# Performance work log

Hardware: AMD Instinct MI355X
Metric: run time of the kernel (lower is better)

The kernel has to match this reference:

```python
import jax, jax.numpy as jnp
import numpy as np

DIM = 512
HEADS = 8
DIM_HEAD = 64
HIDDEN = HEADS * DIM_HEAD
SCALE = DIM_HEAD ** -0.5


def rmsnorm_ch(x, g):
    # F.normalize over channel dim (axis=1), then * g * sqrt(C)
    # x: [b, c, l], g: [c]
    n = jnp.maximum(jnp.linalg.norm(x, axis=1, keepdims=True), 1e-12)
    c = x.shape[1]
    return (x / n) * g[None, :, None] * (c ** 0.5)


def setup_inputs() -> dict:
    key = jax.random.key(0)
    ks = jax.random.split(key, 6)
    b, l = 8, 4096
    x = jax.random.normal(ks[0], (b, DIM, l), dtype=jnp.float32)
    g_in = jnp.ones((DIM,), dtype=jnp.float32)
    # conv1d kernel_size=1 == matmul; kaiming-ish init scale
    w_qkv = jax.random.normal(ks[1], (3 * HIDDEN, DIM), dtype=jnp.float32) * (1.0 / np.sqrt(DIM))
    w_out = jax.random.normal(ks[2], (DIM, HIDDEN), dtype=jnp.float32) * (1.0 / np.sqrt(HIDDEN))
    b_out = jax.random.normal(ks[3], (DIM,), dtype=jnp.float32) * 0.01
    g_out = jnp.ones((DIM,), dtype=jnp.float32)
    return {"x": x, "g_in": g_in, "w_qkv": w_qkv, "w_out": w_out, "b_out": b_out, "g_out": g_out}


def reference(x, g_in, w_qkv, w_out, b_out, g_out):
    b, c, l = x.shape
    residual = x
    xn = rmsnorm_ch(x, g_in)                       # [b, c, l]
    qkv = jnp.einsum('oc,bcl->bol', w_qkv, xn)     # [b, 3*hidden, l]
    q, k, v = jnp.split(qkv, 3, axis=1)            # each [b, hidden, l]
    def to_heads(t):
        return t.reshape(b, HEADS, DIM_HEAD, l)    # [b, h, d, l]
    q, k, v = to_heads(q), to_heads(k), to_heads(v)
    q = jax.nn.softmax(q, axis=2) * SCALE          # softmax over head-dim d
    k = jax.nn.softmax(k, axis=3)                  # softmax over sequence l
    context = jnp.einsum('bhdn,bhen->bhde', k, v)  # [b, h, d, e]
    out = jnp.einsum('bhde,bhdn->bhen', context, q)  # [b, h, e, l]
    out = out.reshape(b, HIDDEN, l)
    o = jnp.einsum('ch,bhl->bcl', w_out, out) + b_out[None, :, None]
    o = rmsnorm_ch(o, g_out)
    return o + residual
```

## Files before the change

### kernel.cpp

```cpp
#include <hip/hip_runtime.h>


#define BB 8
#define CC 512
#define LL 4096
#define HH 8
#define DH 64
#define TC 1536

__device__ __constant__ const float SQRT_C = 22.62741699796952f;
#define SCALE_Q 0.125f

typedef unsigned short bfr_t;
typedef __attribute__((ext_vector_type(8))) short short8;
typedef __attribute__((ext_vector_type(4))) float f32x4;

__device__ __forceinline__ float bf2f(bfr_t v) {
  union { unsigned u; float f; } c; c.u = ((unsigned)v) << 16; return c.f;
}
__device__ __forceinline__ bfr_t f2bf(float f) {
  union { float f; unsigned u; } c; c.f = f;
  unsigned u = c.u + 0x7fffu + ((c.u >> 16) & 1u);
  return (bfr_t)(u >> 16);
}

__device__ __forceinline__ void load_lds16(const bfr_t* g, short* l) {
  __builtin_amdgcn_global_load_lds(
      (const __attribute__((address_space(1))) void*)g,
      (__attribute__((address_space(3))) void*)l, 16, 0, 0);
}

__global__ __launch_bounds__(256) void conv_bf16_2(
    const float* __restrict__ in1, bfr_t* __restrict__ o1, int n1,
    const float* __restrict__ in2, bfr_t* __restrict__ o2, int n2) {
  int i8 = (blockIdx.x * 256 + threadIdx.x) * 8;
  const float* src;
  bfr_t* dst;
  if (i8 < n1) { src = in1 + i8; dst = o1 + i8; }
  else {
    int j8 = i8 - n1;
    if (j8 >= n2) return;
    src = in2 + j8; dst = o2 + j8;
  }
  f32x4 a = *(const f32x4*)src;
  f32x4 b = *(const f32x4*)(src + 4);
  union { short s[8]; f32x4 v; } pk;
#pragma unroll
  for (int u = 0; u < 4; ++u) { pk.s[u] = (short)f2bf(a[u]); pk.s[u + 4] = (short)f2bf(b[u]); }
  *(f32x4*)dst = pk.v;
}

__global__ __launch_bounds__(256) void fused_norm_transpose(
    const float* __restrict__ x, const float* __restrict__ g,
    bfr_t* __restrict__ xt) {
  __shared__ float tile[64][65];
  __shared__ float red[4][64];
  __shared__ float invn_s[64];
  int b = blockIdx.y, l0 = blockIdx.x * 64;
  int t = threadIdx.x, ll = t & 63, cg = t >> 6;
  const float* xb = x + (size_t)b * CC * LL + l0;
  float vals[8][16];
  float ss = 0.f;
#pragma unroll
  for (int ch = 0; ch < 8; ++ch) {
    int c0 = ch * 64;
#pragma unroll
    for (int i = 0; i < 16; ++i) {
      int c = i * 4 + cg;
      float v = xb[(size_t)(c0 + c) * LL + ll];
      vals[ch][i] = v;
      ss += v * v;
    }
  }
  red[cg][ll] = ss;
  __syncthreads();
  if (cg == 0) {
    float s = red[0][ll] + red[1][ll] + red[2][ll] + red[3][ll];
    invn_s[ll] = SQRT_C / fmaxf(sqrtf(s), 1e-12f);
  }
  __syncthreads();
  int lw = t >> 2, ccw = (t & 3) * 16;
  float iv = invn_s[lw];
#pragma unroll
  for (int ch = 0; ch < 8; ++ch) {
    int c0 = ch * 64;
#pragma unroll
    for (int i = 0; i < 16; ++i) tile[i * 4 + cg][ll] = vals[ch][i];
    __syncthreads();
    union { short s[16]; f32x4 v[2]; } pk;
#pragma unroll
    for (int u = 0; u < 16; ++u) {
      int c = ccw + u;
      pk.s[u] = (short)f2bf(tile[c][lw] * g[c0 + c] * iv);
    }
    bfr_t* dst = xt + ((size_t)b * LL + l0 + lw) * CC + c0 + ccw;
    *(f32x4*)dst = pk.v[0];
    *(f32x4*)(dst + 8) = pk.v[1];
    __syncthreads();
  }
}

#define NT 8

__device__ __forceinline__ void stage_half(const bfr_t* g, short* l, int wid) {
  load_lds16(g + (size_t)wid * 8192,        l + wid * 1024);
  load_lds16(g + (size_t)wid * 8192 + 4096, l + wid * 1024 + 512);
}

#define CFENCE asm volatile("" ::: "memory")
#define LGKM0 asm volatile("s_waitcnt lgkmcnt(0)" ::: "memory")
#define VMC0  asm volatile("s_waitcnt vmcnt(0)" ::: "memory")
#define SB    __builtin_amdgcn_sched_barrier(0)
#define BAR   do { CFENCE; __builtin_amdgcn_s_barrier(); CFENCE; } while (0)
#define PRIO1 __builtin_amdgcn_s_setprio(1)
#define PRIO0 __builtin_amdgcn_s_setprio(0)

#define DSR(dst, addr, LIT) \
  asm volatile("ds_read_b128 %0, %1 offset:" #LIT : "=v"(dst) : "v"(addr))

#define RD_A(S, L0, L1, L2, L3) do {           \
    DSR(S[0], aAs0, L0); DSR(S[1], aAs1, L0);  \
    DSR(S[2], aAs0, L1); DSR(S[3], aAs1, L1);  \
    DSR(S[4], aAs0, L2); DSR(S[5], aAs1, L2);  \
    DSR(S[6], aAs0, L3); DSR(S[7], aAs1, L3); } while (0)
#define RD_B(S, L0, L1) do {                   \
    DSR(S[0], bBs0, L0); DSR(S[1], bBs1, L0);  \
    DSR(S[2], bBs0, L1); DSR(S[3], bBs1, L1); } while (0)

#define MMA8(QM, QN, AS, BS) do {                                            \
    _Pragma("unroll") for (int i_ = 0; i_ < 4; ++i_)                         \
      _Pragma("unroll") for (int j_ = 0; j_ < 2; ++j_) {                     \
        acc[(QM)*4+i_][(QN)*2+j_] = __builtin_amdgcn_mfma_f32_16x16x32_bf16( \
            AS[i_*2+0], BS[j_*2+0], acc[(QM)*4+i_][(QN)*2+j_], 0, 0, 0);     \
        acc[(QM)*4+i_][(QN)*2+j_] = __builtin_amdgcn_mfma_f32_16x16x32_bf16( \
            AS[i_*2+1], BS[j_*2+1], acc[(QM)*4+i_][(QN)*2+j_], 0, 0, 0);     \
      }                                                                      \
  } while (0)

#define STAGE_T(J, D) do {                                                   \
    stage_half(pA0 + (J) * 64, As + (D) * 16384, wid);                       \
    stage_half(pA1 + (J) * 64, As + (D) * 16384 + 8192, wid);                \
    stage_half(pB0 + (J) * 64, Bs + (D) * 16384, wid);                       \
    stage_half(pB1 + (J) * 64, Bs + (D) * 16384 + 8192, wid);                \
  } while (0)

#define TILE_E(KT) do {                                                      \
                                      \
    PRIO1; RD_B(bS1, 4096, 6144); MMA8(0, 0, aS0, bS0); PRIO0; LGKM0; SB;    \
                                      \
    PRIO1; RD_A(aS1, 8192, 10240, 12288, 14336); MMA8(0, 1, aS0, bS1);       \
    PRIO0; LGKM0; SB;                                                        \
         \
    if ((KT) < 7) { VMC0; }                                                  \
    BAR;                                                                     \
    if ((KT) <= 5) STAGE_T((KT) + 2, 0);                                     \
    PRIO1;                                                                   \
    if ((KT) < 7) RD_A(aS0, 32768, 34816, 36864, 38912);                     \
    MMA8(1, 1, aS1, bS1); PRIO0; LGKM0; SB;                                  \
            \
    PRIO1; MMA8(1, 0, aS1, bS0); PRIO0;                                      \
    if ((KT) < 7) RD_B(bS0, 32768, 34816);                                   \
    LGKM0; SB;                                                               \
  } while (0)

#define TILE_O(KT) do {                                                      \
    PRIO1; RD_B(bS1, 36864, 38912); MMA8(0, 0, aS0, bS0); PRIO0; LGKM0; SB;  \
    PRIO1; RD_A(aS1, 40960, 43008, 45056, 47104); MMA8(0, 1, aS0, bS1);      \
    PRIO0; LGKM0; SB;                                                        \
    if ((KT) < 7) { VMC0; }                                                  \
    BAR;                                                                     \
    if ((KT) <= 5) STAGE_T((KT) + 2, 1);                                     \
    PRIO1;                                                                   \
    if ((KT) < 7) RD_A(aS0, 0, 2048, 4096, 6144);                            \
    MMA8(1, 1, aS1, bS1); PRIO0; LGKM0; SB;                                  \
    PRIO1; MMA8(1, 0, aS1, bS0); PRIO0;                                      \
    if ((KT) < 7) RD_B(bS0, 0, 2048);                                        \
    LGKM0; SB;                                                               \
  } while (0)

__global__ __launch_bounds__(512, 2) void gemm256(
    const bfr_t* __restrict__ A, const bfr_t* __restrict__ Bt,
    bfr_t* __restrict__ Cout, const float* __restrict__ bias, int M) {
  __shared__ short lds[65536];
  short* As = lds;
  short* Bs = lds + 32768;

  int nwg = gridDim.x;
  int gy = M >> 8;
  int bid = blockIdx.x;
  int logical = (bid & 7) * (nwg >> 3) + (bid >> 3);
  int perz = (LL / 256) * gy;
  int bz = logical / perz;
  int rem = logical - bz * perz;
  int bx = rem / gy;
  int by = rem - bx * gy;

  int m0 = by * 256, n0 = bx * 256;
  int t = threadIdx.x, lane = t & 63, wid = t >> 6;
  int quad = lane >> 4, r16 = lane & 15;
  int wm = wid >> 2, wn = wid & 3;
  int soff = (lane >> 3) * 512 + (((lane & 7) ^ (lane >> 3)) * 8);
  int slot0 = (quad ^ (lane & 7)) * 8;
  int slot1 = ((4 + quad) ^ (lane & 7)) * 8;

  unsigned lb = (unsigned)(uintptr_t)(__attribute__((address_space(3))) short*)lds;
  unsigned aAs0 = lb + (unsigned)(wm * 16384 + r16 * 128 + slot0 * 2);
  unsigned aAs1 = lb + (unsigned)(wm * 16384 + r16 * 128 + slot1 * 2);
  unsigned bbase = 65536u + (unsigned)((wn >> 1) * 16384 + ((wn & 1) * 64 + r16) * 128);
  unsigned bBs0 = lb + bbase + (unsigned)(slot0 * 2);
  unsigned bBs1 = lb + bbase + (unsigned)(slot1 * 2);

  const bfr_t* pA0 = A + (size_t)m0 * 512 + soff;
  const bfr_t* pA1 = pA0 + (size_t)128 * 512;
  const bfr_t* pB0 = Bt + (size_t)bz * LL * 512 + (size_t)n0 * 512 + soff;
  const bfr_t* pB1 = pB0 + (size_t)128 * 512;

  f32x4 acc[8][4] = {};
  short8 aS0[8], aS1[8];
  short8 bS0[4], bS1[4];

  STAGE_T(0, 0);
  STAGE_T(1, 1);
  asm volatile("s_waitcnt vmcnt(8)" ::: "memory");
  BAR;
  RD_A(aS0, 0, 2048, 4096, 6144);
  RD_B(bS0, 0, 2048);
  LGKM0; SB;

  TILE_E(0); TILE_O(1); TILE_E(2); TILE_O(3);
  TILE_E(4); TILE_O(5); TILE_E(6); TILE_O(7);

  bfr_t* Cb = Cout + (size_t)bz * M * LL;
  int crow = m0 + wm * 128 + quad * 4;
  int ccol = n0 + wn * 64 + r16;
#pragma unroll
  for (int am = 0; am < 8; ++am) {
    int rbase = crow + (am >> 2) * 64 + (am & 3) * 16;
#pragma unroll
    for (int reg = 0; reg < 4; ++reg) {
      int row = rbase + reg;
      float bi = bias ? bias[row] : 0.f;
#pragma unroll
      for (int an = 0; an < 4; ++an) {
        int col = ccol + (an >> 1) * 32 + (an & 1) * 16;
        Cb[(size_t)row * LL + col] = f2bf(acc[am][an][reg] + bi);
      }
    }
  }
}

__global__ __launch_bounds__(256) void context_mfma(
    const bfr_t* __restrict__ qkv, float* __restrict__ ctx_p,
    float* __restrict__ ksum_p) {
  __shared__ float red[4][4096];
  int s = blockIdx.x, bh = blockIdx.y;
  int b = bh >> 3, h = bh & 7;
  int t = threadIdx.x, lane = t & 63, wid = t >> 6;
  int quad = lane >> 4, r = lane & 15;
  const bfr_t* kb = qkv + ((size_t)b * TC + 512 + h * 64) * LL;
  const bfr_t* vb = qkv + ((size_t)b * TC + 1024 + h * 64) * LL;
  int n_base = s * 512 + wid * 128;
  f32x4 acc[4][4] = {};
  float ps[4] = {};
#pragma unroll
  for (int ks = 0; ks < 4; ++ks) {
    int n0 = n_base + ks * 32;
    short8 af[4], bf8[4];
#pragma unroll
    for (int i = 0; i < 4; ++i) {
      union { short s[8]; short8 v8; } uk;
      uk.v8 = *(const short8*)&kb[(size_t)(i * 16 + r) * LL + n0 + quad * 8];
#pragma unroll
      for (int jj = 0; jj < 8; ++jj) {
        float e = __expf(bf2f((bfr_t)uk.s[jj]));
        uk.s[jj] = (short)f2bf(e);
        ps[i] += e;
      }
      af[i] = uk.v8;
      bf8[i] = *(const short8*)&vb[(size_t)(i * 16 + r) * LL + n0 + quad * 8];
    }
#pragma unroll
    for (int i = 0; i < 4; ++i)
#pragma unroll
      for (int j = 0; j < 4; ++j)
        acc[i][j] = __builtin_amdgcn_mfma_f32_16x16x32_bf16(af[i], bf8[j],
                                                            acc[i][j], 0, 0, 0);
  }
#pragma unroll
  for (int i = 0; i < 4; ++i) {
    ps[i] += __shfl_xor(ps[i], 16, 64);
    ps[i] += __shfl_xor(ps[i], 32, 64);
  }
  if (quad == 0) {
#pragma unroll
    for (int i = 0; i < 4; ++i) red[wid][i * 16 + r] = ps[i];
  }
  __syncthreads();
  if (t < 64)
    ksum_p[((size_t)bh * 8 + s) * 64 + t] =
        red[0][t] + red[1][t] + red[2][t] + red[3][t];
  __syncthreads();
#pragma unroll
  for (int i = 0; i < 4; ++i)
#pragma unroll
    for (int j = 0; j < 4; ++j)
#pragma unroll
      for (int reg = 0; reg < 4; ++reg)
        red[wid][(i * 16 + quad * 4 + reg) * 64 + j * 16 + r] = acc[i][j][reg];
  __syncthreads();
  float* out = ctx_p + ((size_t)bh * 8 + s) * 4096;
#pragma unroll
  for (int u = 0; u < 16; ++u) {
    int idx = u * 256 + t;
    out[idx] = red[0][idx] + red[1][idx] + red[2][idx] + red[3][idx];
  }
}

__global__ __launch_bounds__(256) void context_reduce(
    const float* __restrict__ ctx_p, const float* __restrict__ ksum_p,
    bfr_t* __restrict__ ctx_bf) {
  __shared__ float zinv[64];
  int bh = blockIdx.x;
  int t = threadIdx.x;
  if (t < 64) {
    float s = 0.f;
#pragma unroll
    for (int s8 = 0; s8 < 8; ++s8) s += ksum_p[((size_t)bh * 8 + s8) * 64 + t];
    zinv[t] = 1.f / s;
  }
  __syncthreads();
#pragma unroll
  for (int i = 0; i < 16; ++i) {
    int idx = i * 256 + t;
    int d = idx >> 6;
    float sum = 0.f;
#pragma unroll
    for (int s = 0; s < 8; ++s) sum += ctx_p[((size_t)bh * 8 + s) * 4096 + idx];
    ctx_bf[(size_t)bh * 4096 + idx] = f2bf(sum * zinv[d]);
  }
}

__global__ __launch_bounds__(256) void apply_fused(
    const bfr_t* __restrict__ qkv, const bfr_t* __restrict__ ctx_bf,
    bfr_t* __restrict__ out_t) {
  int b = blockIdx.z, h = blockIdx.y;
  int t = threadIdx.x, lane = t & 63, wid = t >> 6;
  int quad = lane >> 4, r = lane & 15;
  int n0 = blockIdx.x * 256 + wid * 64;
  const bfr_t* qb = qkv + ((size_t)b * TC + h * 64) * LL;
  const bfr_t* cb = ctx_bf + (size_t)(b * HH + h) * 4096;
  float v[4][16];
  float pm[4];
#pragma unroll
  for (int i = 0; i < 4; ++i) {
    pm[i] = -1e30f;
#pragma unroll
    for (int ks = 0; ks < 2; ++ks)
#pragma unroll
      for (int jj = 0; jj < 8; ++jj) {
        float q = bf2f(qb[(size_t)(ks * 32 + quad * 8 + jj) * LL + n0 + i * 16 + r]);
        v[i][ks * 8 + jj] = q;
        pm[i] = fmaxf(pm[i], q);
      }
  }
#pragma unroll
  for (int i = 0; i < 4; ++i) {
    pm[i] = fmaxf(pm[i], __shfl_xor(pm[i], 16, 64));
    pm[i] = fmaxf(pm[i], __shfl_xor(pm[i], 32, 64));
  }
  float psum[4];
#pragma unroll
  for (int i = 0; i < 4; ++i) {
    float s = 0.f;
#pragma unroll
    for (int u = 0; u < 16; ++u) { v[i][u] = __expf(v[i][u] - pm[i]); s += v[i][u]; }
    psum[i] = s;
  }
#pragma unroll
  for (int i = 0; i < 4; ++i) {
    psum[i] += __shfl_xor(psum[i], 16, 64);
    psum[i] += __shfl_xor(psum[i], 32, 64);
  }
  short8 af[2][4];
#pragma unroll
  for (int i = 0; i < 4; ++i) {
    float sc = SCALE_Q / psum[i];
#pragma unroll
    for (int ks = 0; ks < 2; ++ks) {
      union { short s[8]; short8 v8; } u;
#pragma unroll
      for (int jj = 0; jj < 8; ++jj) u.s[jj] = (short)f2bf(v[i][ks * 8 + jj] * sc);
      af[ks][i] = u.v8;
    }
  }
  short8 bfrag[2][4];
#pragma unroll
  for (int ks = 0; ks < 2; ++ks)
#pragma unroll
    for (int j = 0; j < 4; ++j) {
      union { short s[8]; short8 v8; } u;
#pragma unroll
      for (int jj = 0; jj < 8; ++jj)
        u.s[jj] = (short)cb[(ks * 32 + quad * 8 + jj) * 64 + j * 16 + r];
      bfrag[ks][j] = u.v8;
    }
  f32x4 acc[4][4] = {};
#pragma unroll
  for (int ks = 0; ks < 2; ++ks)
#pragma unroll
    for (int i = 0; i < 4; ++i)
#pragma unroll
      for (int j = 0; j < 4; ++j)
        acc[i][j] = __builtin_amdgcn_mfma_f32_16x16x32_bf16(af[ks][i], bfrag[ks][j],
                                                            acc[i][j], 0, 0, 0);
  bfr_t* dst = out_t + (size_t)b * LL * 512 + h * 64;
#pragma unroll
  for (int i = 0; i < 4; ++i)
#pragma unroll
    for (int reg = 0; reg < 4; ++reg) {
      int row = n0 + i * 16 + quad * 4 + reg;
#pragma unroll
      for (int j = 0; j < 4; ++j)
        dst[(size_t)row * 512 + j * 16 + r] = f2bf(acc[i][j][reg]);
    }
}

__global__ __launch_bounds__(256) void final_norm_res(
    const bfr_t* __restrict__ o, const float* __restrict__ g,
    const float* __restrict__ x, float* __restrict__ out) {
  __shared__ float red[4][64];
  __shared__ float invn[64];
  int b = blockIdx.y, l0 = blockIdx.x * 64;
  int t = threadIdx.x, ll = t & 63, cg = t >> 6;
  const bfr_t* ob = o + (size_t)b * CC * LL + l0 + ll;
  unsigned pk[64];
  float ss = 0.f;
#pragma unroll
  for (int i = 0; i < 64; ++i) {
    int c = cg * 128 + 2 * i;
    unsigned u0 = ob[(size_t)c * LL];
    unsigned u1 = ob[(size_t)(c + 1) * LL];
    float v0 = bf2f((bfr_t)u0), v1 = bf2f((bfr_t)u1);
    ss += v0 * v0 + v1 * v1;
    pk[i] = u0 | (u1 << 16);
  }
  red[cg][ll] = ss;
  __syncthreads();
  if (cg == 0) {
    float s = red[0][ll] + red[1][ll] + red[2][ll] + red[3][ll];
    invn[ll] = SQRT_C / fmaxf(sqrtf(s), 1e-12f);
  }
  __syncthreads();
  float iv = invn[ll];
  const float* xb = x + (size_t)b * CC * LL + l0 + ll;
  float* outb = out + (size_t)b * CC * LL + l0 + ll;
#pragma unroll
  for (int i = 0; i < 64; ++i) {
    int c = cg * 128 + 2 * i;
    float v0 = bf2f((bfr_t)(pk[i] & 0xffffu));
    float v1 = bf2f((bfr_t)(pk[i] >> 16));
    outb[(size_t)c * LL] = v0 * g[c] * iv + xb[(size_t)c * LL];
    outb[(size_t)(c + 1) * LL] = v1 * g[c + 1] * iv + xb[(size_t)(c + 1) * LL];
  }
}

extern "C" void kernel_launch(void* const* d_in, const int* in_sizes, int n_in,
                              void* d_out, int out_size, void* d_ws,
                              size_t ws_size, hipStream_t stream) {
  const float* x     = (const float*)d_in[0];
  const float* g_in  = (const float*)d_in[1];
  const float* w_qkv = (const float*)d_in[2];
  const float* w_out = (const float*)d_in[3];
  const float* b_out = (const float*)d_in[4];
  const float* g_out = (const float*)d_in[5];
  float* out = (float*)d_out;

  char* ws = (char*)d_ws;
  const size_t off_wqkv  = 0;
  const size_t off_wout  = 1572864;
  const size_t off_ksump = 2097152;
  const size_t off_ctx   = 2260992;
  const size_t off_ctxp  = 3309568;
  const size_t off_xt    = 11698176;
  const size_t off_qkv   = 45252608;
  const size_t ws_need   = 145915904;
  if (ws_size < ws_need) return;

  bfr_t* wqkv_bf = (bfr_t*)(ws + off_wqkv);
  bfr_t* wout_bf = (bfr_t*)(ws + off_wout);
  float* ksum_p  = (float*)(ws + off_ksump);
  bfr_t* ctx_bf  = (bfr_t*)(ws + off_ctx);
  float* ctxp    = (float*)(ws + off_ctxp);
  bfr_t* xt      = (bfr_t*)(ws + off_xt);
  bfr_t* qkv     = (bfr_t*)(ws + off_qkv);
  bfr_t* o_bf    = (bfr_t*)(ws + off_qkv);

  conv_bf16_2<<<dim3((1536 * 512 + 512 * 512) / 8 / 256), 256, 0, stream>>>(
      w_qkv, wqkv_bf, 1536 * 512, w_out, wout_bf, 512 * 512);
  fused_norm_transpose<<<dim3(LL / 64, BB), 256, 0, stream>>>(x, g_in, xt);
  gemm256<<<dim3((LL / 256) * (TC / 256) * BB), 512, 0, stream>>>(wqkv_bf, xt, qkv, nullptr, TC);
  context_mfma<<<dim3(8, BB * HH), 256, 0, stream>>>(qkv, ctxp, ksum_p);
  context_reduce<<<dim3(BB * HH), 256, 0, stream>>>(ctxp, ksum_p, ctx_bf);
  apply_fused<<<dim3(LL / 256, HH, BB), 256, 0, stream>>>(qkv, ctx_bf, xt);
  gemm256<<<dim3((LL / 256) * (CC / 256) * BB), 512, 0, stream>>>(wout_bf, xt, o_bf, b_out, CC);
  final_norm_res<<<dim3(LL / 64, BB), 256, 0, stream>>>(o_bf, g_out, x, out);
}
```

Before: 280.9 us.

## Split QKV GEMM into three launches, drop softmax max pass, widen final norm

New measurement: 299.2 us. 1.07x slower.

```diff
diff --git a/kernel.cpp b/kernel.cpp
--- a/kernel.cpp
+++ b/kernel.cpp
@@ -145,19 +145,15 @@
   } while (0)
 
 #define TILE_E(KT) do {                                                      \
-                                      \
     PRIO1; RD_B(bS1, 4096, 6144); MMA8(0, 0, aS0, bS0); PRIO0; LGKM0; SB;    \
-                                      \
-    PRIO1; RD_A(aS1, 8192, 10240, 12288, 14336); MMA8(0, 1, aS0, bS1);       \
+    PRIO1; RD_A(aS1, 8192, 10240, 12288, 14336); MMA8(0, 1, aS0, bS1);      \
     PRIO0; LGKM0; SB;                                                        \
-         \
     if ((KT) < 7) { VMC0; }                                                  \
     BAR;                                                                     \
     if ((KT) <= 5) STAGE_T((KT) + 2, 0);                                     \
     PRIO1;                                                                   \
     if ((KT) < 7) RD_A(aS0, 32768, 34816, 36864, 38912);                     \
     MMA8(1, 1, aS1, bS1); PRIO0; LGKM0; SB;                                  \
-            \
     PRIO1; MMA8(1, 0, aS1, bS0); PRIO0;                                      \
     if ((KT) < 7) RD_B(bS0, 32768, 34816);                                   \
     LGKM0; SB;                                                               \
@@ -165,7 +161,7 @@
 
 #define TILE_O(KT) do {                                                      \
     PRIO1; RD_B(bS1, 36864, 38912); MMA8(0, 0, aS0, bS0); PRIO0; LGKM0; SB;  \
-    PRIO1; RD_A(aS1, 40960, 43008, 45056, 47104); MMA8(0, 1, aS0, bS1);      \
+    PRIO1; RD_A(aS1, 40960, 43008, 45056, 47104); MMA8(0, 1, aS0, bS1);     \
     PRIO0; LGKM0; SB;                                                        \
     if ((KT) < 7) { VMC0; }                                                  \
     BAR;                                                                     \
@@ -180,7 +176,7 @@
 
 __global__ __launch_bounds__(512, 2) void gemm256(
     const bfr_t* __restrict__ A, const bfr_t* __restrict__ Bt,
-    bfr_t* __restrict__ Cout, const float* __restrict__ bias, int M) {
+    bfr_t* __restrict__ Cout, const float* __restrict__ bias, int M, int Mtot) {
   __shared__ short lds[65536];
   short* As = lds;
   short* Bs = lds + 32768;
@@ -230,7 +226,7 @@
   TILE_E(0); TILE_O(1); TILE_E(2); TILE_O(3);
   TILE_E(4); TILE_O(5); TILE_E(6); TILE_O(7);
 
-  bfr_t* Cb = Cout + (size_t)bz * M * LL;
+  bfr_t* Cb = Cout + (size_t)bz * Mtot * LL;
   int crow = m0 + wm * 128 + quad * 4;
   int ccol = n0 + wn * 64 + r16;
 #pragma unroll
@@ -350,30 +346,19 @@
   const bfr_t* qb = qkv + ((size_t)b * TC + h * 64) * LL;
   const bfr_t* cb = ctx_bf + (size_t)(b * HH + h) * 4096;
   float v[4][16];
-  float pm[4];
+  float psum[4];
 #pragma unroll
   for (int i = 0; i < 4; ++i) {
-    pm[i] = -1e30f;
+    float s = 0.f;
 #pragma unroll
     for (int ks = 0; ks < 2; ++ks)
 #pragma unroll
       for (int jj = 0; jj < 8; ++jj) {
         float q = bf2f(qb[(size_t)(ks * 32 + quad * 8 + jj) * LL + n0 + i * 16 + r]);
-        v[i][ks * 8 + jj] = q;
-        pm[i] = fmaxf(pm[i], q);
+        float e = __expf(q);
+        v[i][ks * 8 + jj] = e;
+        s += e;
       }
-  }
-#pragma unroll
-  for (int i = 0; i < 4; ++i) {
-    pm[i] = fmaxf(pm[i], __shfl_xor(pm[i], 16, 64));
-    pm[i] = fmaxf(pm[i], __shfl_xor(pm[i], 32, 64));
-  }
-  float psum[4];
-#pragma unroll
-  for (int i = 0; i < 4; ++i) {
-    float s = 0.f;
-#pragma unroll
-    for (int u = 0; u < 16; ++u) { v[i][u] = __expf(v[i][u] - pm[i]); s += v[i][u]; }
     psum[i] = s;
   }
 #pragma unroll
@@ -428,39 +413,40 @@
 __global__ __launch_bounds__(256) void final_norm_res(
     const bfr_t* __restrict__ o, const float* __restrict__ g,
     const float* __restrict__ x, float* __restrict__ out) {
-  __shared__ float red[4][64];
-  __shared__ float invn[64];
-  int b = blockIdx.y, l0 = blockIdx.x * 64;
+  __shared__ float red[4][128];
+  __shared__ float invn[128];
+  int b = blockIdx.y, l0 = blockIdx.x * 128;
   int t = threadIdx.x, ll = t & 63, cg = t >> 6;
-  const bfr_t* ob = o + (size_t)b * CC * LL + l0 + ll;
-  unsigned pk[64];
-  float ss = 0.f;
-#pragma unroll
-  for (int i = 0; i < 64; ++i) {
-    int c = cg * 128 + 2 * i;
-    unsigned u0 = ob[(size_t)c * LL];
-    unsigned u1 = ob[(size_t)(c + 1) * LL];
-    float v0 = bf2f((bfr_t)u0), v1 = bf2f((bfr_t)u1);
-    ss += v0 * v0 + v1 * v1;
-    pk[i] = u0 | (u1 << 16);
-  }
-  red[cg][ll] = ss;
-  __syncthreads();
-  if (cg == 0) {
-    float s = red[0][ll] + red[1][ll] + red[2][ll] + red[3][ll];
-    invn[ll] = SQRT_C / fmaxf(sqrtf(s), 1e-12f);
-  }
-  __syncthreads();
-  float iv = invn[ll];
-  const float* xb = x + (size_t)b * CC * LL + l0 + ll;
-  float* outb = out + (size_t)b * CC * LL + l0 + ll;
-#pragma unroll
-  for (int i = 0; i < 64; ++i) {
-    int c = cg * 128 + 2 * i;
-    float v0 = bf2f((bfr_t)(pk[i] & 0xffffu));
-    float v1 = bf2f((bfr_t)(pk[i] >> 16));
-    outb[(size_t)c * LL] = v0 * g[c] * iv + xb[(size_t)c * LL];
-    outb[(size_t)(c + 1) * LL] = v1 * g[c + 1] * iv + xb[(size_t)(c + 1) * LL];
+  const bfr_t* ob = o + (size_t)b * CC * LL + l0 + ll * 2;
+  float ss0 = 0.f, ss1 = 0.f;
+  for (int c = cg * 128; c < cg * 128 + 128; ++c) {
+    unsigned u = *(const unsigned*)&ob[(size_t)c * LL];
+    float v0 = bf2f((bfr_t)(u & 0xffffu));
+    float v1 = bf2f((bfr_t)(u >> 16));
+    ss0 += v0 * v0;
+    ss1 += v1 * v1;
+  }
+  red[cg][ll * 2] = ss0;
+  red[cg][ll * 2 + 1] = ss1;
+  __syncthreads();
+  if (t < 128) {
+    float s = red[0][t] + red[1][t] + red[2][t] + red[3][t];
+    invn[t] = SQRT_C / fmaxf(sqrtf(s), 1e-12f);
+  }
+  __syncthreads();
+  float iv0 = invn[ll * 2], iv1 = invn[ll * 2 + 1];
+  const float* xb = x + (size_t)b * CC * LL + l0 + ll * 2;
+  float* outb = out + (size_t)b * CC * LL + l0 + ll * 2;
+  for (int c = cg * 128; c < cg * 128 + 128; ++c) {
+    unsigned u = *(const unsigned*)&ob[(size_t)c * LL];
+    float gc = g[c];
+    float v0 = bf2f((bfr_t)(u & 0xffffu)) * gc * iv0;
+    float v1 = bf2f((bfr_t)(u >> 16)) * gc * iv1;
+    float2 xv = *(const float2*)&xb[(size_t)c * LL];
+    float2 ov;
+    ov.x = v0 + xv.x;
+    ov.y = v1 + xv.y;
+    *(float2*)&outb[(size_t)c * LL] = ov;
   }
 }
 
@@ -498,10 +484,13 @@
   conv_bf16_2<<<dim3((1536 * 512 + 512 * 512) / 8 / 256), 256, 0, stream>>>(
       w_qkv, wqkv_bf, 1536 * 512, w_out, wout_bf, 512 * 512);
   fused_norm_transpose<<<dim3(LL / 64, BB), 256, 0, stream>>>(x, g_in, xt);
-  gemm256<<<dim3((LL / 256) * (TC / 256) * BB), 512, 0, stream>>>(wqkv_bf, xt, qkv, nullptr, TC);
+  for (int p = 0; p < 3; ++p)
+    gemm256<<<dim3((LL / 256) * 2 * BB), 512, 0, stream>>>(
+        wqkv_bf + (size_t)p * 512 * 512, xt, qkv + (size_t)p * 512 * LL,
+        nullptr, 512, TC);
   context_mfma<<<dim3(8, BB * HH), 256, 0, stream>>>(qkv, ctxp, ksum_p);
   context_reduce<<<dim3(BB * HH), 256, 0, stream>>>(ctxp, ksum_p, ctx_bf);
   apply_fused<<<dim3(LL / 256, HH, BB), 256, 0, stream>>>(qkv, ctx_bf, xt);
-  gemm256<<<dim3((LL / 256) * (CC / 256) * BB), 512, 0, stream>>>(wout_bf, xt, o_bf, b_out, CC);
-  final_norm_res<<<dim3(LL / 64, BB), 256, 0, stream>>>(o_bf, g_out, x, out);
-}
+  gemm256<<<dim3((LL / 256) * 2 * BB), 512, 0, stream>>>(wout_bf, xt, o_bf, b_out, 512, 512);
+  final_norm_res<<<dim3(LL / 128, BB), 256, 0, stream>>>(o_bf, g_out, x, out);
+}
```
